# Kernel optimization log

Measured on AMD Instinct MI355X. Metric: run time of the kernel, lower is better.

The kernel has to match this reference:

```python
import jax, jax.numpy as jnp
import numpy as np

TEMP = 0.05
EPS = 1e-8  # torch CosineSimilarity default eps


def _normalize(x):
    # torch cosine_similarity clamps norm at eps
    n = jnp.maximum(jnp.linalg.norm(x, axis=-1, keepdims=True), EPS)
    return x / n


def setup_inputs() -> dict:
    key = jax.random.key(0)
    k1, k2, k3 = jax.random.split(key, 3)
    N, D = 4096, 1024
    return {
        "repr_sent": jax.random.normal(k1, (N, D), dtype=jnp.float32),
        "repr_pos": jax.random.normal(k2, (N, D), dtype=jnp.float32),
        "repr_neg": jax.random.normal(k3, (N, D), dtype=jnp.float32),
    }


def reference(repr_sent, repr_pos, repr_neg):
    # Normalize then GEMM instead of broadcasting an [N, 2N, D] intermediate.
    s = _normalize(repr_sent)            # [N, D]
    p = _normalize(repr_pos)             # [N, D]
    n = _normalize(repr_neg)             # [N, D]
    cand = jnp.concatenate([p, n], axis=0)           # [2N, D]
    sim = jnp.einsum("nd,md->nm", s, cand) / TEMP    # [N, 2N]
    # Cross-entropy with labels = arange(N) (positive is the i-th column)
    logz = jax.nn.logsumexp(sim, axis=-1)            # [N]
    N_ = sim.shape[0]
    pos_logit = jnp.diagonal(sim[:, :N_])            # sim[i, i]
    loss = jnp.mean(logz - pos_logit)
    return loss
```

## Files before the change

### kernel.cpp

```cpp
#include <hip/hip_runtime.h>
#include <stdint.h>

#define N_ROWS 4096
#define D_DIM  1024
#define N_CAND 8192
#define TEMP_INV 20.0f
#define QSCALE 508.0f
#define OUT_SCALE (TEMP_INV / (QSCALE * QSCALE))

#define BM 256
#define BN 256
#define BK 64
#define NT 16

typedef __attribute__((ext_vector_type(4))) int i32x4;

using gvoid = __attribute__((address_space(1))) void;
using lvoid = __attribute__((address_space(3))) void;

#define BAR() __builtin_amdgcn_s_barrier()
#define SCHED0() __builtin_amdgcn_sched_barrier(0)

__global__ __launch_bounds__(256) void prep_kernel(
    const float* __restrict__ s, const float* __restrict__ p,
    const float* __restrict__ ng, unsigned char* __restrict__ s_q,
    unsigned char* __restrict__ cand_q, float* __restrict__ rowsum) {
  const int row = blockIdx.x;
  const int t = threadIdx.x;
  const float* src;
  unsigned char* dst;
  if (row < N_ROWS) {
    src = s + (size_t)row * D_DIM;
    dst = s_q + (size_t)row * D_DIM;
  } else if (row < 2 * N_ROWS) {
    src = p + (size_t)(row - N_ROWS) * D_DIM;
    dst = cand_q + (size_t)(row - N_ROWS) * D_DIM;
  } else {
    src = ng + (size_t)(row - 2 * N_ROWS) * D_DIM;
    dst = cand_q + (size_t)(row - N_ROWS) * D_DIM;
  }

  float4 v = reinterpret_cast<const float4*>(src)[t];
  float ss = v.x * v.x + v.y * v.y + v.z * v.z + v.w * v.w;
#pragma unroll
  for (int m = 32; m >= 1; m >>= 1) ss += __shfl_xor(ss, m, 64);
  __shared__ float red[4];
  const int w = t >> 6, l = t & 63;
  if (l == 0) red[w] = ss;
  __syncthreads();
  const float tot = red[0] + red[1] + red[2] + red[3];
  const float qs = QSCALE / fmaxf(sqrtf(tot), 1e-8f);

  auto q8 = [&](float x) -> unsigned {
    return (unsigned)((int)rintf(fminf(fmaxf(x * qs, -127.0f), 127.0f))) &
           0xffu;
  };
  const unsigned pk =
      q8(v.x) | (q8(v.y) << 8) | (q8(v.z) << 16) | (q8(v.w) << 24);
  *reinterpret_cast<unsigned*>(dst + t * 4) = pk;

  if (t == 0 && row < N_ROWS) rowsum[row] = 0.0f;
}

__global__ __launch_bounds__(1024) void gemm_lse_kernel(
    const unsigned char* __restrict__ s_q,
    const unsigned char* __restrict__ cand_q,
    float* __restrict__ rowsum, float* __restrict__ pos) {
  __shared__ __align__(16) unsigned char lds[4 * 32768];

  const int t = threadIdx.x;
  const int w = t >> 6;
  const int l = t & 63;
  const int g = l >> 4;
  const int rl = l & 15;
  const int wm = w >> 2;
  const int wn = w & 3;
  const int slot = (g + (rl >> 1)) & 3;
  const int rowBase = blockIdx.y * BM;
  const int colBase = blockIdx.x * BN;

  i32x4 acc[4][4] = {};
  i32x4 af[4];
  i32x4 bf[4];

  const int sRow = t >> 2;
  const int sSlotL = ((t & 3) - (t >> 3)) & 3;
  const unsigned char* gA =
      s_q + (size_t)(rowBase + sRow) * D_DIM + sSlotL * 16;
  const unsigned char* gB =
      cand_q + (size_t)(colBase + sRow) * D_DIM + sSlotL * 16;

  auto stage = [&](int T) {
    const int buf = (T & 3) * 32768;
    const size_t ko = (size_t)T * 64;
    __builtin_amdgcn_global_load_lds((const gvoid*)(gA + ko),
                                     (lvoid*)(lds + buf + t * 16), 16, 0, 0);
    __builtin_amdgcn_global_load_lds(
        (const gvoid*)(gB + ko),
        (lvoid*)(lds + buf + 16384 + t * 16), 16, 0, 0);
  };

  stage(0); stage(1);
  asm volatile("s_waitcnt vmcnt(2)" ::: "memory");
  SCHED0();
  BAR(); SCHED0();

  for (int T = 0; T < NT; ++T) {
    const unsigned char* A = lds + (T & 3) * 32768;
    const unsigned char* B = A + 16384;
#pragma unroll
    for (int m = 0; m < 4; ++m) {
      const int r = wm * 64 + m * 16 + rl;
      af[m] = *reinterpret_cast<const i32x4*>(A + r * 64 + slot * 16);
    }
#pragma unroll
    for (int n = 0; n < 4; ++n) {
      const int r = wn * 64 + n * 16 + rl;
      bf[n] = *reinterpret_cast<const i32x4*>(B + r * 64 + slot * 16);
    }
    if (T + 2 < NT) stage(T + 2);

    __builtin_amdgcn_s_setprio(1);
#pragma unroll
    for (int m = 0; m < 4; ++m)
#pragma unroll
      for (int n = 0; n < 4; ++n)
        acc[m][n] = __builtin_amdgcn_mfma_i32_16x16x64_i8(
            af[m], bf[n], acc[m][n], 0, 0, 0);
    __builtin_amdgcn_s_setprio(0);

    if (T + 2 < NT) {
      asm volatile("s_waitcnt vmcnt(2)" ::: "memory");
    } else if (T == NT - 2) {
      asm volatile("s_waitcnt vmcnt(0)" ::: "memory");
    }
    SCHED0();
    BAR(); SCHED0();
  }

  __syncthreads();
  float* red = reinterpret_cast<float*>(lds);
  if (t < BM) red[t] = 0.0f;
  __syncthreads();

#pragma unroll
  for (int m = 0; m < 4; ++m) {
#pragma unroll
    for (int j = 0; j < 4; ++j) {
      const int rloc = wm * 64 + m * 16 + g * 4 + j;
      const int rowg = rowBase + rloc;
      float sm = 0.0f;
#pragma unroll
      for (int n = 0; n < 4; ++n) {
        const int colg = colBase + wn * 64 + n * 16 + rl;
        const float simv = (float)acc[m][n][j] * OUT_SCALE;
        if (colg == rowg) pos[rowg] = simv;
        sm += __expf(simv - TEMP_INV);
      }
      sm += __shfl_xor(sm, 1, 64);
      sm += __shfl_xor(sm, 2, 64);
      sm += __shfl_xor(sm, 4, 64);
      sm += __shfl_xor(sm, 8, 64);
      if (rl == 0) atomicAdd(&red[rloc], sm);
    }
  }
  __syncthreads();
  if (t < BM) atomicAdd(&rowsum[rowBase + t], red[t]);
}

__global__ __launch_bounds__(1024) void loss_kernel(
    const float* __restrict__ rowsum, const float* __restrict__ pos,
    float* __restrict__ out) {
  const int t = threadIdx.x;
  float acc = 0.0f;
  for (int i = t; i < N_ROWS; i += 1024)
    acc += TEMP_INV + logf(rowsum[i]) - pos[i];
#pragma unroll
  for (int m = 32; m >= 1; m >>= 1) acc += __shfl_xor(acc, m, 64);
  __shared__ float red[16];
  const int w = t >> 6, l = t & 63;
  if (l == 0) red[w] = acc;
  __syncthreads();
  if (t == 0) {
    float tot = 0.0f;
#pragma unroll
    for (int i = 0; i < 16; ++i) tot += red[i];
    out[0] = tot / (float)N_ROWS;
  }
}

extern "C" void kernel_launch(void* const* d_in, const int* in_sizes, int n_in,
                              void* d_out, int out_size, void* d_ws,
                              size_t ws_size, hipStream_t stream) {
  (void)in_sizes; (void)n_in; (void)out_size; (void)ws_size;
  const float* s = (const float*)d_in[0];
  const float* p = (const float*)d_in[1];
  const float* ng = (const float*)d_in[2];

  unsigned char* s_q = (unsigned char*)d_ws;
  unsigned char* cand_q = s_q + (size_t)N_ROWS * D_DIM;
  float* rowsum = (float*)(cand_q + (size_t)N_CAND * D_DIM);
  float* pos = rowsum + N_ROWS;
  float* out = (float*)d_out;

  prep_kernel<<<dim3(3 * N_ROWS), dim3(256), 0, stream>>>(s, p, ng, s_q,
                                                          cand_q, rowsum);
  gemm_lse_kernel<<<dim3(N_CAND / BN, N_ROWS / BM), dim3(1024), 0, stream>>>(
      s_q, cand_q, rowsum, pos);
  loss_kernel<<<dim3(1), dim3(1024), 0, stream>>>(rowsum, pos, out);
}
```

Measured before the change: 58.64 us.

## Shrink GEMM block to 128x256 with 512 threads and software-pipelined fragment loads

Halves the row tile and the thread count (8 waves, each still computing 64x64), so LDS per block drops from 128KB to 96KB. It moves to a 3-deep global→LDS prefetch and double-buffers register fragments, so the next tile's LDS reads are interleaved with the current tile's MFMA groups. The goal is to hide LDS read latency behind MFMA work and to launch twice as many blocks for better CU occupancy. In exchange it adds more block-level atomics into rowsum and more complex waitcnt bookkeeping, which could be fragile.

New measurement: 70.62 us. 20.4% more time.

```diff
diff --git a/kernel.cpp b/kernel.cpp
--- a/kernel.cpp
+++ b/kernel.cpp
@@ -8,10 +8,11 @@
 #define QSCALE 508.0f
 #define OUT_SCALE (TEMP_INV / (QSCALE * QSCALE))
 
-#define BM 256
+#define BM 128
 #define BN 256
 #define BK 64
 #define NT 16
+#define BUFSZ 24576
 
 typedef __attribute__((ext_vector_type(4))) int i32x4;
 
@@ -62,11 +63,11 @@
   if (t == 0 && row < N_ROWS) rowsum[row] = 0.0f;
 }
 
-__global__ __launch_bounds__(1024) void gemm_lse_kernel(
+__global__ __launch_bounds__(512) void gemm_lse_kernel(
     const unsigned char* __restrict__ s_q,
     const unsigned char* __restrict__ cand_q,
     float* __restrict__ rowsum, float* __restrict__ pos) {
-  __shared__ __align__(16) unsigned char lds[4 * 32768];
+  __shared__ __align__(16) unsigned char lds[4 * BUFSZ];
 
   const int t = threadIdx.x;
   const int w = t >> 6;
@@ -79,63 +80,106 @@
   const int rowBase = blockIdx.y * BM;
   const int colBase = blockIdx.x * BN;
 
+  const int aOff = wm * 4096 + rl * 64 + slot * 16;
+  const int bOff = 8192 + wn * 4096 + rl * 64 + slot * 16;
+
   i32x4 acc[4][4] = {};
-  i32x4 af[4];
-  i32x4 bf[4];
-
-  const int sRow = t >> 2;
+  i32x4 afA[4], bfA[4];
+  i32x4 afB[4], bfB[4];
+
   const int sSlotL = ((t & 3) - (t >> 3)) & 3;
   const unsigned char* gA =
-      s_q + (size_t)(rowBase + sRow) * D_DIM + sSlotL * 16;
+      s_q + (size_t)(rowBase + (t >> 2)) * D_DIM + sSlotL * 16;
   const unsigned char* gB =
-      cand_q + (size_t)(colBase + sRow) * D_DIM + sSlotL * 16;
+      cand_q + (size_t)(colBase + (t >> 2)) * D_DIM + sSlotL * 16;
 
   auto stage = [&](int T) {
-    const int buf = (T & 3) * 32768;
+    const int buf = (T & 3) * BUFSZ;
     const size_t ko = (size_t)T * 64;
     __builtin_amdgcn_global_load_lds((const gvoid*)(gA + ko),
                                      (lvoid*)(lds + buf + t * 16), 16, 0, 0);
     __builtin_amdgcn_global_load_lds(
         (const gvoid*)(gB + ko),
+        (lvoid*)(lds + buf + 8192 + t * 16), 16, 0, 0);
+    __builtin_amdgcn_global_load_lds(
+        (const gvoid*)(gB + ko + (size_t)128 * D_DIM),
         (lvoid*)(lds + buf + 16384 + t * 16), 16, 0, 0);
   };
 
-  stage(0); stage(1);
-  asm volatile("s_waitcnt vmcnt(2)" ::: "memory");
+  auto tile_step = [&](int T, i32x4 (&cAf)[4], i32x4 (&cBf)[4],
+                       i32x4 (&nAf)[4], i32x4 (&nBf)[4]) {
+    if (T + 3 < NT) stage(T + 3);
+    const bool rd = (T + 1 < NT);
+    const unsigned char* nb = lds + ((T + 1) & 3) * BUFSZ;
+
+    if (rd) { nAf[0] = *reinterpret_cast<const i32x4*>(nb + aOff);
+              nAf[1] = *reinterpret_cast<const i32x4*>(nb + aOff + 1024); }
+    SCHED0();
+    __builtin_amdgcn_s_setprio(1);
+#pragma unroll
+    for (int n = 0; n < 4; ++n)
+      acc[0][n] = __builtin_amdgcn_mfma_i32_16x16x64_i8(cAf[0], cBf[n],
+                                                        acc[0][n], 0, 0, 0);
+    __builtin_amdgcn_s_setprio(0);
+    SCHED0();
+
+    if (rd) { nAf[2] = *reinterpret_cast<const i32x4*>(nb + aOff + 2048);
+              nAf[3] = *reinterpret_cast<const i32x4*>(nb + aOff + 3072); }
+    SCHED0();
+    __builtin_amdgcn_s_setprio(1);
+#pragma unroll
+    for (int n = 0; n < 4; ++n)
+      acc[1][n] = __builtin_amdgcn_mfma_i32_16x16x64_i8(cAf[1], cBf[n],
+                                                        acc[1][n], 0, 0, 0);
+    __builtin_amdgcn_s_setprio(0);
+    SCHED0();
+
+    if (rd) { nBf[0] = *reinterpret_cast<const i32x4*>(nb + bOff);
+              nBf[1] = *reinterpret_cast<const i32x4*>(nb + bOff + 1024); }
+    SCHED0();
+    __builtin_amdgcn_s_setprio(1);
+#pragma unroll
+    for (int n = 0; n < 4; ++n)
+      acc[2][n] = __builtin_amdgcn_mfma_i32_16x16x64_i8(cAf[2], cBf[n],
+                                                        acc[2][n], 0, 0, 0);
+    __builtin_amdgcn_s_setprio(0);
+    SCHED0();
+
+    if (rd) { nBf[2] = *reinterpret_cast<const i32x4*>(nb + bOff + 2048);
+              nBf[3] = *reinterpret_cast<const i32x4*>(nb + bOff + 3072); }
+    SCHED0();
+    __builtin_amdgcn_s_setprio(1);
+#pragma unroll
+    for (int n = 0; n < 4; ++n)
+      acc[3][n] = __builtin_amdgcn_mfma_i32_16x16x64_i8(cAf[3], cBf[n],
+                                                        acc[3][n], 0, 0, 0);
+    __builtin_amdgcn_s_setprio(0);
+    SCHED0();
+
+    if (T <= NT - 4) {
+      asm volatile("s_waitcnt vmcnt(3)" ::: "memory");
+    } else if (T == NT - 3) {
+      asm volatile("s_waitcnt vmcnt(0)" ::: "memory");
+    }
+    SCHED0();
+    if (T + 1 < NT) { BAR(); SCHED0(); }
+  };
+
+  stage(0); stage(1); stage(2);
+  asm volatile("s_waitcnt vmcnt(3)" ::: "memory");
   SCHED0();
   BAR(); SCHED0();
 
-  for (int T = 0; T < NT; ++T) {
-    const unsigned char* A = lds + (T & 3) * 32768;
-    const unsigned char* B = A + 16384;
-#pragma unroll
-    for (int m = 0; m < 4; ++m) {
-      const int r = wm * 64 + m * 16 + rl;
-      af[m] = *reinterpret_cast<const i32x4*>(A + r * 64 + slot * 16);
-    }
-#pragma unroll
-    for (int n = 0; n < 4; ++n) {
-      const int r = wn * 64 + n * 16 + rl;
-      bf[n] = *reinterpret_cast<const i32x4*>(B + r * 64 + slot * 16);
-    }
-    if (T + 2 < NT) stage(T + 2);
-
-    __builtin_amdgcn_s_setprio(1);
-#pragma unroll
-    for (int m = 0; m < 4; ++m)
-#pragma unroll
-      for (int n = 0; n < 4; ++n)
-        acc[m][n] = __builtin_amdgcn_mfma_i32_16x16x64_i8(
-            af[m], bf[n], acc[m][n], 0, 0, 0);
-    __builtin_amdgcn_s_setprio(0);
-
-    if (T + 2 < NT) {
-      asm volatile("s_waitcnt vmcnt(2)" ::: "memory");
-    } else if (T == NT - 2) {
-      asm volatile("s_waitcnt vmcnt(0)" ::: "memory");
-    }
-    SCHED0();
-    BAR(); SCHED0();
+#pragma unroll
+  for (int m = 0; m < 4; ++m)
+    afA[m] = *reinterpret_cast<const i32x4*>(lds + aOff + m * 1024);
+#pragma unroll
+  for (int n = 0; n < 4; ++n)
+    bfA[n] = *reinterpret_cast<const i32x4*>(lds + bOff + n * 1024);
+
+  for (int it = 0; it < NT / 2; ++it) {
+    tile_step(2 * it, afA, bfA, afB, bfB);
+    tile_step(2 * it + 1, afB, bfB, afA, bfA);
   }
 
   __syncthreads();
@@ -205,7 +249,7 @@
 
   prep_kernel<<<dim3(3 * N_ROWS), dim3(256), 0, stream>>>(s, p, ng, s_q,
                                                           cand_q, rowsum);
-  gemm_lse_kernel<<<dim3(N_CAND / BN, N_ROWS / BM), dim3(1024), 0, stream>>>(
+  gemm_lse_kernel<<<dim3(N_CAND / BN, N_ROWS / BM), dim3(512), 0, stream>>>(
       s_q, cand_q, rowsum, pos);
   loss_kernel<<<dim3(1), dim3(1024), 0, stream>>>(rowsum, pos, out);
 }
```
